# Kernel tuning notes

Hardware: AMD Instinct MI355X
Metric: run time of the kernel (lower is better)

## Reference

```python
import jax, jax.numpy as jnp
import numpy as np


def setup_inputs() -> dict:
    key = jax.random.key(0)
    P, B, S = 128, 128, 4096
    k1, k2, k3, k4 = jax.random.split(key, 4)
    # SPD inducing Gram K_ii
    A = jax.random.normal(k1, (P, 2 * P), jnp.float32)
    K_ii = A @ A.T / (2.0 * P) + 1e-2 * jnp.eye(P, dtype=jnp.float32)
    # cross-covariances [B, S, P]
    K_ti = jax.random.normal(k2, (B, S, P), jnp.float32) * 0.1
    # diagonal K_t must dominate the quadratic form so the Schur complement is positive
    Kii_inv = jnp.linalg.inv(K_ii)
    qf = jnp.einsum('bsp,pq,bsq->bs', K_ti, Kii_inv, K_ti)
    K_t = qf + jax.random.uniform(k3, (B, S), jnp.float32) + 0.1
    # learned parameters
    V = jax.random.normal(k4, (P, P), jnp.float32) / jnp.sqrt(P) + jnp.eye(P, dtype=jnp.float32)
    latent_Gscale = jnp.zeros((), jnp.float32)
    dof = 128
    return dict(K_ii=K_ii, K_ti=K_ti, K_t=K_t, V=V, latent_Gscale=latent_Gscale, dof=dof)


def reference(K_ii, K_ti, K_t, V, latent_Gscale, dof):
    P = K_ii.shape[0]
    ti = K_ti.reshape(-1, P)          # [N, P]
    tt = K_t.reshape(-1)              # [N]
    # pos_inv via Cholesky (SPD inverse)
    L = jnp.linalg.cholesky(K_ii)
    Kii_inv = jax.scipy.linalg.cho_solve((L, True), jnp.eye(P, dtype=K_ii.dtype))
    A = ti @ Kii_inv                  # Kti_inv_Kii_flat, [N, P]
    ktt_i = tt - jnp.sum(A * ti, -1)  # Schur complement diag
    # G = V V^T / P * exp(scale)
    G = (V @ V.T) / V.shape[1] * jnp.exp(latent_Gscale)
    Gti = A @ G                       # [N, P]
    gt = jnp.sum(Gti * A, -1) + ktt_i
    # objective: -0.5 * dof * (-(logdet G + logdet Kinv) + tr(Kinv G) - P)
    trace_term = jnp.sum(Kii_inv * G.T)
    logdet_G = jnp.linalg.slogdet(G)[1]
    logdet_Kinv = -2.0 * jnp.sum(jnp.log(jnp.diag(L)))
    obj = -0.5 * dof * (-(logdet_G + logdet_Kinv) + trace_term - P)
    Gii = G
    return (Gii, Gti.reshape(K_ti.shape), gt.reshape(K_t.shape), obj)
```

## Files before the change

### kernel.cpp

```cpp
#include <hip/hip_runtime.h>
#include <cstdint>

typedef __attribute__((ext_vector_type(8))) short short8;
typedef __attribute__((ext_vector_type(4))) float f32x4;

__device__ __forceinline__ unsigned short f2bf(float f) {
    uint32_t u = __builtin_bit_cast(uint32_t, f);
    u += 0x7FFFu + ((u >> 16) & 1u);
    return (unsigned short)(u >> 16);
}

#define SG_OFF   16384
#define SM1_OFF  32768
#define SY_OFF   49152
#define SX_OFF   65536
#define SD_OFF   81920

__global__ __launch_bounds__(256) void k0_G(
    const float* __restrict__ V, const float* __restrict__ gs,
    float* __restrict__ out)
{
    float* sG = out + SG_OFF;
    const float egs = expf(gs[0]) * (1.0f / 128.0f);
    const int ty = threadIdx.x >> 5, tx = threadIdx.x & 31;
    const int r = blockIdx.x * 8 + ty;
    const f32x4* V4 = (const f32x4*)V;
    f32x4 acc = {0.f, 0.f, 0.f, 0.f};
    for (int kq = 0; kq < 32; ++kq) {
        const f32x4 vr = V4[r * 32 + kq];
        #pragma unroll
        for (int e = 0; e < 4; ++e) {
            const f32x4 vc = V4[(tx * 4 + e) * 32 + kq];
            acc[e] += vr[0]*vc[0] + vr[1]*vc[1] + vr[2]*vc[2] + vr[3]*vc[3];
        }
    }
    acc *= egs;
    *(f32x4*)&out[r * 128 + tx * 4] = acc;
    *(f32x4*)&sG[r * 128 + tx * 4] = acc;
}

__global__ __launch_bounds__(512, 2) void k1_factor(
    const float* __restrict__ Kii, float* __restrict__ out)
{
    __shared__ float colA[2][128], colB[2][128], rowX[2][128];
    __shared__ float sDk[128], sDg[128], sRed[4];

    const int tid = threadIdx.x;
    const int ty = tid >> 5, tx = tid & 31;
    const int I0 = ty * 8, J0 = tx * 4;
    const float* sG = out + SG_OFF;
    float* sX = out + SX_OFF;
    float* dbuf = out + SD_OFF;

    f32x4 rA[8], rB[8], rX[8];
    #pragma unroll
    for (int r = 0; r < 8; ++r) {
        rA[r] = *(const f32x4*)&Kii[(size_t)(I0 + r) * 128 + J0];
        rB[r] = *(const f32x4*)&sG[(I0 + r) * 128 + J0];
        f32x4 z = {0.f, 0.f, 0.f, 0.f};
        #pragma unroll
        for (int e = 0; e < 4; ++e) z[e] = (I0 + r == J0 + e) ? 1.0f : 0.0f;
        rX[r] = z;
    }
    if (tx == 0) {
        #pragma unroll
        for (int r = 0; r < 8; ++r) { colA[0][I0 + r] = rA[r][0]; colB[0][I0 + r] = rB[r][0]; }
    }
    if (ty == 0) {
        #pragma unroll
        for (int e = 0; e < 4; ++e) rowX[0][J0 + e] = rX[0][e];
    }
    __syncthreads();

    for (int k = 0; k < 127; ++k) {
        const int b = k & 1;
        const float dK = colA[b][k], dG = colB[b][k];
        const float rdK = 1.0f / dK, rdG = 1.0f / dG;
        if (tid == 0) { sDk[k] = dK; sDg[k] = dG; }

        f32x4 caj = *(const f32x4*)&colA[b][J0];
        f32x4 cbj = *(const f32x4*)&colB[b][J0];
        const f32x4 xj = *(const f32x4*)&rowX[b][J0];
        #pragma unroll
        for (int e = 0; e < 4; ++e)
            if (J0 + e <= k) { caj[e] = 0.0f; cbj[e] = 0.0f; }

        f32x4 ca0 = *(const f32x4*)&colA[b][I0];
        f32x4 ca1 = *(const f32x4*)&colA[b][I0 + 4];
        f32x4 cb0 = *(const f32x4*)&colB[b][I0];
        f32x4 cb1 = *(const f32x4*)&colB[b][I0 + 4];
        #pragma unroll
        for (int r = 0; r < 4; ++r) {
            if (I0 + r <= k)     { ca0[r] = 0.0f; cb0[r] = 0.0f; }
            if (I0 + 4 + r <= k) { ca1[r] = 0.0f; cb1[r] = 0.0f; }
        }

        if (I0 + 7 > k) {
            #pragma unroll
            for (int r = 0; r < 8; ++r) {
                const float am = (r < 4) ? ca0[r & 3] : ca1[r & 3];
                const float bm = (r < 4) ? cb0[r & 3] : cb1[r & 3];
                const float fA = am * rdK;
                const float fB = bm * rdG;
                rA[r] -= fA * caj;
                rB[r] -= fB * cbj;
                rX[r] -= fA * xj;
            }
        }

        const int kn = k + 1, bn = kn & 1;
        if (tx == (kn >> 2)) {
            const int es = kn & 3;
            #pragma unroll
            for (int ee = 0; ee < 4; ++ee) if (ee == es) {
                #pragma unroll
                for (int r = 0; r < 8; ++r) {
                    colA[bn][I0 + r] = rA[r][ee];
                    colB[bn][I0 + r] = rB[r][ee];
                }
            }
        }
        if (ty == (kn >> 3)) {
            const int rs = kn & 7;
            #pragma unroll
            for (int rr = 0; rr < 8; ++rr) if (rr == rs) {
                #pragma unroll
                for (int e = 0; e < 4; ++e) rowX[bn][J0 + e] = rX[rr][e];
            }
        }
        __syncthreads();
    }
    if (tid == 511) { sDk[127] = rA[7][3]; sDg[127] = rB[7][3]; }

    #pragma unroll
    for (int r = 0; r < 8; ++r)
        *(f32x4*)&sX[(I0 + r) * 128 + J0] = rX[r];
    __syncthreads();

    if (tid < 128) {
        dbuf[tid] = sDk[tid];
        float lk = logf(sDk[tid]);
        float lg = logf(sDg[tid]);
        #pragma unroll
        for (int o = 32; o > 0; o >>= 1) { lk += __shfl_xor(lk, o, 64); lg += __shfl_xor(lg, o, 64); }
        if ((tid & 63) == 0) { sRed[(tid >> 6) * 2] = lk; sRed[(tid >> 6) * 2 + 1] = lg; }
    }
    __syncthreads();
    if (tid == 0) {
        dbuf[128] = sRed[0] + sRed[2];
        dbuf[129] = sRed[1] + sRed[3];
    }
}

__global__ __launch_bounds__(256) void k2_M1(float* __restrict__ out)
{
    const float* sX = out + SX_OFF;
    const float* dbuf = out + SD_OFF;
    float* sM1 = out + SM1_OFF;
    __shared__ float srd[128];
    const int tid = threadIdx.x;
    if (tid < 128) srd[tid] = 1.0f / dbuf[tid];
    __syncthreads();
    const int ty = tid >> 5, tx = tid & 31;
    const int a = blockIdx.x * 8 + ty;
    const f32x4* X4 = (const f32x4*)sX;
    f32x4 acc = {0.f, 0.f, 0.f, 0.f};
    for (int k = a; k < 128; ++k) {
        const float xa = sX[k * 128 + a] * srd[k];
        acc += xa * X4[k * 32 + tx];
    }
    *(f32x4*)&sM1[a * 128 + tx * 4] = acc;
}

__global__ __launch_bounds__(256) void k3_Y(float* __restrict__ out, char* __restrict__ wsb)
{
    const float* sG = out + SG_OFF;
    const float* sM1 = out + SM1_OFF;
    float* sY = out + SY_OFF;
    float* dbuf = out + SD_OFF;
    const int tid = threadIdx.x;
    const int ty = tid >> 5, tx = tid & 31;
    const int c = blockIdx.x * 8 + ty;
    const f32x4* M14 = (const f32x4*)sM1;
    f32x4 acc = {0.f, 0.f, 0.f, 0.f};
    for (int m = 0; m < 128; ++m)
        acc += sG[c * 128 + m] * M14[m * 32 + tx];
    *(f32x4*)&sY[c * 128 + tx * 4] = acc;
    const uint32_t lo = (uint32_t)f2bf(acc[0]) | ((uint32_t)f2bf(acc[1]) << 16);
    const uint32_t hi = (uint32_t)f2bf(acc[2]) | ((uint32_t)f2bf(acc[3]) << 16);
    const uint32_t byteoff = (uint32_t)((c * 256 + tx * 8) ^ ((c & 7) << 4));
    *(uint2*)(wsb + byteoff) = make_uint2(lo, hi);
    float t;
    {
        const f32x4* G4 = (const f32x4*)sG;
        const int idx = blockIdx.x * 256 + tid;
        const f32x4 g = G4[idx], mm = M14[idx];
        t = g[0]*mm[0] + g[1]*mm[1] + g[2]*mm[2] + g[3]*mm[3];
    }
    #pragma unroll
    for (int o = 32; o > 0; o >>= 1) t += __shfl_xor(t, o, 64);
    __shared__ float sp[4];
    if ((tid & 63) == 0) sp[tid >> 6] = t;
    __syncthreads();
    if (tid == 0) dbuf[132 + blockIdx.x] = sp[0] + sp[1] + sp[2] + sp[3];
}

__global__ __launch_bounds__(256) void k4_Q(
    float* __restrict__ out, char* __restrict__ wsb, const int* __restrict__ dofp)
{
    const float* sM1 = out + SM1_OFF;
    const float* sY = out + SY_OFF;
    const float* dbuf = out + SD_OFF;
    const int tid = threadIdx.x;
    const int ty = tid >> 5, tx = tid & 31;
    const int c = blockIdx.x * 8 + ty;
    const f32x4* Y4 = (const f32x4*)sY;
    const f32x4* M14 = (const f32x4*)sM1;
    f32x4 acc = -M14[c * 32 + tx];
    for (int m = 0; m < 128; ++m)
        acc += sM1[c * 128 + m] * Y4[m * 32 + tx];
    const uint32_t lo = (uint32_t)f2bf(acc[0]) | ((uint32_t)f2bf(acc[1]) << 16);
    const uint32_t hi = (uint32_t)f2bf(acc[2]) | ((uint32_t)f2bf(acc[3]) << 16);
    const uint32_t byteoff = (uint32_t)((c * 256 + tx * 8) ^ ((c & 7) << 4));
    *(uint2*)(wsb + 32768 + byteoff) = make_uint2(lo, hi);
    if (blockIdx.x == 0 && tid == 0) {
        float trace = 0.0f;
        for (int i = 0; i < 16; ++i) trace += dbuf[132 + i];
        const float ldK = dbuf[128], ldG = dbuf[129];
        const float dof = (float)dofp[0];
        out[67649536] = -0.5f * dof * (-(ldG - ldK) + trace - 128.0f);
    }
}

__global__ __launch_bounds__(512) void main_kernel(
    const float* __restrict__ Kti, const float* __restrict__ Kt,
    const float* __restrict__ ws, float* __restrict__ Gti,
    float* __restrict__ gt)
{
    __shared__ __align__(16) char smem[65536];
    const int tid = threadIdx.x;
    const int lane = tid & 63, wid = tid >> 6;
    const int l15 = lane & 15, l4 = lane >> 4;
    const int brow = blockIdx.x * 256;
    const int wrow = wid * 32;

    const float* tbase = Kti + (size_t)(brow + wrow + l15) * 128;

    f32x4 t[4][4];
    #pragma unroll
    for (int kc = 0; kc < 4; ++kc) {
        const float* p0 = tbase + kc * 32 + l4 * 8;
        const float* p1 = p0 + 16 * 128;
        t[kc][0] = *(const f32x4*)p0;
        t[kc][1] = *(const f32x4*)(p0 + 4);
        t[kc][2] = *(const f32x4*)p1;
        t[kc][3] = *(const f32x4*)(p1 + 4);
    }

    {
        f32x4* s4 = (f32x4*)smem;
        const f32x4* w4 = (const f32x4*)ws;
        #pragma unroll
        for (int i = 0; i < 8; ++i) s4[tid + i * 512] = w4[tid + i * 512];
    }

    short8 a[4][2];
    #pragma unroll
    for (int kc = 0; kc < 4; ++kc) {
        a[kc][0] = { (short)f2bf(t[kc][0][0]), (short)f2bf(t[kc][0][1]), (short)f2bf(t[kc][0][2]), (short)f2bf(t[kc][0][3]),
                     (short)f2bf(t[kc][1][0]), (short)f2bf(t[kc][1][1]), (short)f2bf(t[kc][1][2]), (short)f2bf(t[kc][1][3]) };
        a[kc][1] = { (short)f2bf(t[kc][2][0]), (short)f2bf(t[kc][2][1]), (short)f2bf(t[kc][2][2]), (short)f2bf(t[kc][2][3]),
                     (short)f2bf(t[kc][3][0]), (short)f2bf(t[kc][3][1]), (short)f2bf(t[kc][3][2]), (short)f2bf(t[kc][3][3]) };
    }
    __syncthreads();

    f32x4 accW[2][8] = {};
    f32x4 accZ[2][8] = {};
    #pragma unroll
    for (int kc = 0; kc < 4; ++kc) {
        const int k0 = kc * 32 + l4 * 8;
        #pragma unroll
        for (int ct = 0; ct < 8; ++ct) {
            const int c = ct * 16 + l15;
            const int byteoff = (c * 256 + k0 * 2) ^ ((c & 7) << 4);
            const short8 bW = *(const short8*)(smem + byteoff);
            const short8 bQ = *(const short8*)(smem + 32768 + byteoff);
            accW[0][ct] = __builtin_amdgcn_mfma_f32_16x16x32_bf16(a[kc][0], bW, accW[0][ct], 0, 0, 0);
            accW[1][ct] = __builtin_amdgcn_mfma_f32_16x16x32_bf16(a[kc][1], bW, accW[1][ct], 0, 0, 0);
            accZ[0][ct] = __builtin_amdgcn_mfma_f32_16x16x32_bf16(a[kc][0], bQ, accZ[0][ct], 0, 0, 0);
            accZ[1][ct] = __builtin_amdgcn_mfma_f32_16x16x32_bf16(a[kc][1], bQ, accZ[1][ct], 0, 0, 0);
        }
    }

    #pragma unroll
    for (int rt = 0; rt < 2; ++rt) {
        #pragma unroll
        for (int r = 0; r < 4; ++r) {
            const int row = brow + wrow + rt * 16 + l4 * 4 + r;
            const float* trow = Kti + (size_t)row * 128;
            float p = 0.0f;
            #pragma unroll
            for (int ct = 0; ct < 8; ++ct) p += accZ[rt][ct][r] * trow[ct * 16 + l15];
            p += __shfl_xor(p, 1, 64);
            p += __shfl_xor(p, 2, 64);
            p += __shfl_xor(p, 4, 64);
            p += __shfl_xor(p, 8, 64);
            if (l15 == 0) gt[row] = Kt[row] + p;
        }
    }

    #pragma unroll
    for (int rt = 0; rt < 2; ++rt) {
        #pragma unroll
        for (int r = 0; r < 4; ++r) {
            float* grow = Gti + (size_t)(brow + wrow + rt * 16 + l4 * 4 + r) * 128 + l15;
            #pragma unroll
            for (int ct = 0; ct < 8; ++ct)
                grow[ct * 16] = accW[rt][ct][r];
        }
    }
}

extern "C" void kernel_launch(void* const* d_in, const int* in_sizes, int n_in,
                              void* d_out, int out_size, void* d_ws, size_t ws_size,
                              hipStream_t stream)
{
    const float* Kii = (const float*)d_in[0];
    const float* Kti = (const float*)d_in[1];
    const float* Kt  = (const float*)d_in[2];
    const float* V   = (const float*)d_in[3];
    const float* gs  = (const float*)d_in[4];
    const int*   dof = (const int*)d_in[5];
    float* out = (float*)d_out;
    float* ws  = (float*)d_ws;

    const int N = in_sizes[2];
    const int nblocks = N / 256;

    k0_G<<<16, 256, 0, stream>>>(V, gs, out);
    k1_factor<<<1, 512, 0, stream>>>(Kii, out);
    k2_M1<<<16, 256, 0, stream>>>(out);
    k3_Y<<<16, 256, 0, stream>>>(out, (char*)ws);
    k4_Q<<<16, 256, 0, stream>>>(out, (char*)ws, dof);
    main_kernel<<<nblocks, 512, 0, stream>>>(Kti, Kt, ws,
                                             out + 16384,
                                             out + 67125248);
}
```

Baseline: 306.2 us.

## Fuse G computation into factor kernel and merge M1/Y/Q kernels into one

Computes G = V V^T scaled inside the single-block factorization kernel, and merges the M1, Y and Q matrix products plus the trace reduction into one 16-block kernel that keeps M1 in shared memory. This removes three kernel launches and the global-memory staging of intermediate matrices. In exchange, each block redundantly recomputes the full M1, and the single-block factor kernel does extra serial work to form G.

```diff
diff --git a/kernel.cpp b/kernel.cpp
--- a/kernel.cpp
+++ b/kernel.cpp
@@ -10,37 +10,12 @@
     return (unsigned short)(u >> 16);
 }
 
-#define SG_OFF   16384
-#define SM1_OFF  32768
-#define SY_OFF   49152
 #define SX_OFF   65536
 #define SD_OFF   81920
 
-__global__ __launch_bounds__(256) void k0_G(
-    const float* __restrict__ V, const float* __restrict__ gs,
-    float* __restrict__ out)
-{
-    float* sG = out + SG_OFF;
-    const float egs = expf(gs[0]) * (1.0f / 128.0f);
-    const int ty = threadIdx.x >> 5, tx = threadIdx.x & 31;
-    const int r = blockIdx.x * 8 + ty;
-    const f32x4* V4 = (const f32x4*)V;
-    f32x4 acc = {0.f, 0.f, 0.f, 0.f};
-    for (int kq = 0; kq < 32; ++kq) {
-        const f32x4 vr = V4[r * 32 + kq];
-        #pragma unroll
-        for (int e = 0; e < 4; ++e) {
-            const f32x4 vc = V4[(tx * 4 + e) * 32 + kq];
-            acc[e] += vr[0]*vc[0] + vr[1]*vc[1] + vr[2]*vc[2] + vr[3]*vc[3];
-        }
-    }
-    acc *= egs;
-    *(f32x4*)&out[r * 128 + tx * 4] = acc;
-    *(f32x4*)&sG[r * 128 + tx * 4] = acc;
-}
-
-__global__ __launch_bounds__(512, 2) void k1_factor(
-    const float* __restrict__ Kii, float* __restrict__ out)
+__global__ __launch_bounds__(512, 2) void kA_factor(
+    const float* __restrict__ Kii, const float* __restrict__ V,
+    const float* __restrict__ gscale, float* __restrict__ out)
 {
     __shared__ float colA[2][128], colB[2][128], rowX[2][128];
     __shared__ float sDk[128], sDg[128], sRed[4];
@@ -48,15 +23,39 @@
     const int tid = threadIdx.x;
     const int ty = tid >> 5, tx = tid & 31;
     const int I0 = ty * 8, J0 = tx * 4;
-    const float* sG = out + SG_OFF;
     float* sX = out + SX_OFF;
     float* dbuf = out + SD_OFF;
 
-    f32x4 rA[8], rB[8], rX[8];
+    f32x4 rB[8];
+    {
+        const float egs = expf(gscale[0]) * (1.0f / 128.0f);
+        const f32x4* V4 = (const f32x4*)V;
+        float acc[8][4] = {};
+        for (int q = 0; q < 32; ++q) {
+            f32x4 vc[4];
+            #pragma unroll
+            for (int e = 0; e < 4; ++e) vc[e] = V4[(J0 + e) * 32 + q];
+            #pragma unroll
+            for (int r = 0; r < 8; ++r) {
+                const f32x4 vr = V4[(I0 + r) * 32 + q];
+                #pragma unroll
+                for (int e = 0; e < 4; ++e)
+                    acc[r][e] += vr[0]*vc[e][0] + vr[1]*vc[e][1]
+                               + vr[2]*vc[e][2] + vr[3]*vc[e][3];
+            }
+        }
+        #pragma unroll
+        for (int r = 0; r < 8; ++r) {
+            const f32x4 g = { acc[r][0]*egs, acc[r][1]*egs, acc[r][2]*egs, acc[r][3]*egs };
+            rB[r] = g;
+            *(f32x4*)&out[(I0 + r) * 128 + J0] = g;
+        }
+    }
+
+    f32x4 rA[8], rX[8];
     #pragma unroll
     for (int r = 0; r < 8; ++r) {
         rA[r] = *(const f32x4*)&Kii[(size_t)(I0 + r) * 128 + J0];
-        rB[r] = *(const f32x4*)&sG[(I0 + r) * 128 + J0];
         f32x4 z = {0.f, 0.f, 0.f, 0.f};
         #pragma unroll
         for (int e = 0; e < 4; ++e) z[e] = (I0 + r == J0 + e) ? 1.0f : 0.0f;
@@ -152,83 +151,96 @@
     }
 }
 
-__global__ __launch_bounds__(256) void k2_M1(float* __restrict__ out)
-{
-    const float* sX = out + SX_OFF;
-    const float* dbuf = out + SD_OFF;
-    float* sM1 = out + SM1_OFF;
-    __shared__ float srd[128];
-    const int tid = threadIdx.x;
-    if (tid < 128) srd[tid] = 1.0f / dbuf[tid];
-    __syncthreads();
-    const int ty = tid >> 5, tx = tid & 31;
-    const int a = blockIdx.x * 8 + ty;
-    const f32x4* X4 = (const f32x4*)sX;
-    f32x4 acc = {0.f, 0.f, 0.f, 0.f};
-    for (int k = a; k < 128; ++k) {
-        const float xa = sX[k * 128 + a] * srd[k];
-        acc += xa * X4[k * 32 + tx];
-    }
-    *(f32x4*)&sM1[a * 128 + tx * 4] = acc;
-}
-
-__global__ __launch_bounds__(256) void k3_Y(float* __restrict__ out, char* __restrict__ wsb)
-{
-    const float* sG = out + SG_OFF;
-    const float* sM1 = out + SM1_OFF;
-    float* sY = out + SY_OFF;
-    float* dbuf = out + SD_OFF;
-    const int tid = threadIdx.x;
-    const int ty = tid >> 5, tx = tid & 31;
-    const int c = blockIdx.x * 8 + ty;
-    const f32x4* M14 = (const f32x4*)sM1;
-    f32x4 acc = {0.f, 0.f, 0.f, 0.f};
-    for (int m = 0; m < 128; ++m)
-        acc += sG[c * 128 + m] * M14[m * 32 + tx];
-    *(f32x4*)&sY[c * 128 + tx * 4] = acc;
-    const uint32_t lo = (uint32_t)f2bf(acc[0]) | ((uint32_t)f2bf(acc[1]) << 16);
-    const uint32_t hi = (uint32_t)f2bf(acc[2]) | ((uint32_t)f2bf(acc[3]) << 16);
-    const uint32_t byteoff = (uint32_t)((c * 256 + tx * 8) ^ ((c & 7) << 4));
-    *(uint2*)(wsb + byteoff) = make_uint2(lo, hi);
-    float t;
-    {
-        const f32x4* G4 = (const f32x4*)sG;
-        const int idx = blockIdx.x * 256 + tid;
-        const f32x4 g = G4[idx], mm = M14[idx];
-        t = g[0]*mm[0] + g[1]*mm[1] + g[2]*mm[2] + g[3]*mm[3];
-    }
-    #pragma unroll
-    for (int o = 32; o > 0; o >>= 1) t += __shfl_xor(t, o, 64);
-    __shared__ float sp[4];
-    if ((tid & 63) == 0) sp[tid >> 6] = t;
-    __syncthreads();
-    if (tid == 0) dbuf[132 + blockIdx.x] = sp[0] + sp[1] + sp[2] + sp[3];
-}
-
-__global__ __launch_bounds__(256) void k4_Q(
+__global__ __launch_bounds__(256) void kG_rest(
     float* __restrict__ out, char* __restrict__ wsb, const int* __restrict__ dofp)
 {
-    const float* sM1 = out + SM1_OFF;
-    const float* sY = out + SY_OFF;
+    __shared__ float M1s[128 * 132];
+    __shared__ float Zs[8 * 132];
+    __shared__ float srd[128];
+
+    const int tid = threadIdx.x;
+    const int bid = blockIdx.x;
+    const float* Xg = out + SX_OFF;
     const float* dbuf = out + SD_OFF;
-    const int tid = threadIdx.x;
-    const int ty = tid >> 5, tx = tid & 31;
-    const int c = blockIdx.x * 8 + ty;
-    const f32x4* Y4 = (const f32x4*)sY;
-    const f32x4* M14 = (const f32x4*)sM1;
-    f32x4 acc = -M14[c * 32 + tx];
-    for (int m = 0; m < 128; ++m)
-        acc += sM1[c * 128 + m] * Y4[m * 32 + tx];
-    const uint32_t lo = (uint32_t)f2bf(acc[0]) | ((uint32_t)f2bf(acc[1]) << 16);
-    const uint32_t hi = (uint32_t)f2bf(acc[2]) | ((uint32_t)f2bf(acc[3]) << 16);
-    const uint32_t byteoff = (uint32_t)((c * 256 + tx * 8) ^ ((c & 7) << 4));
-    *(uint2*)(wsb + 32768 + byteoff) = make_uint2(lo, hi);
-    if (blockIdx.x == 0 && tid == 0) {
-        float trace = 0.0f;
-        for (int i = 0; i < 16; ++i) trace += dbuf[132 + i];
-        const float ldK = dbuf[128], ldG = dbuf[129];
-        const float dof = (float)dofp[0];
-        out[67649536] = -0.5f * dof * (-(ldG - ldK) + trace - 128.0f);
+    const float* G = out;
+
+    if (tid < 128) srd[tid] = 1.0f / dbuf[tid];
+    __syncthreads();
+
+    {
+        const int ty = tid >> 5, tx = tid & 31;
+        const int I0 = ty * 16, J0 = tx * 4;
+        f32x4 acc[16] = {};
+        for (int k = 0; k < 128; ++k) {
+            f32x4 xb = *(const f32x4*)&Xg[k * 128 + J0];
+            xb *= srd[k];
+            const f32x4 xa0 = *(const f32x4*)&Xg[k * 128 + I0];
+            const f32x4 xa1 = *(const f32x4*)&Xg[k * 128 + I0 + 4];
+            const f32x4 xa2 = *(const f32x4*)&Xg[k * 128 + I0 + 8];
+            const f32x4 xa3 = *(const f32x4*)&Xg[k * 128 + I0 + 12];
+            #pragma unroll
+            for (int r = 0; r < 4; ++r) {
+                acc[r]      += xa0[r] * xb;
+                acc[r + 4]  += xa1[r] * xb;
+                acc[r + 8]  += xa2[r] * xb;
+                acc[r + 12] += xa3[r] * xb;
+            }
+        }
+        #pragma unroll
+        for (int r = 0; r < 16; ++r)
+            *(f32x4*)&M1s[(I0 + r) * 132 + J0] = acc[r];
+    }
+    __syncthreads();
+
+    const int r8 = tid >> 5;
+    const int j4 = tid & 31;
+    const int c = bid * 8 + r8;
+
+    {
+        f32x4 y = {0.f, 0.f, 0.f, 0.f};
+        const float* grow = G + (size_t)c * 128;
+        for (int m = 0; m < 128; ++m)
+            y += grow[m] * *(const f32x4*)&M1s[m * 132 + j4 * 4];
+        const uint32_t lo = (uint32_t)f2bf(y[0]) | ((uint32_t)f2bf(y[1]) << 16);
+        const uint32_t hi = (uint32_t)f2bf(y[2]) | ((uint32_t)f2bf(y[3]) << 16);
+        const uint32_t byteoff = (uint32_t)((c * 256 + j4 * 8) ^ ((c & 7) << 4));
+        *(uint2*)(wsb + byteoff) = make_uint2(lo, hi);
+    }
+
+    float trp = 0.0f;
+    {
+        f32x4 z = {0.f, 0.f, 0.f, 0.f};
+        const f32x4* G4 = (const f32x4*)G;
+        for (int m = 0; m < 128; ++m) {
+            const f32x4 g = G4[m * 32 + j4];
+            z += M1s[c * 132 + m] * g;
+            if (r8 == 0) {
+                const f32x4 mm = *(const f32x4*)&M1s[m * 132 + j4 * 4];
+                trp += mm[0]*g[0] + mm[1]*g[1] + mm[2]*g[2] + mm[3]*g[3];
+            }
+        }
+        *(f32x4*)&Zs[r8 * 132 + j4 * 4] = z;
+    }
+    __syncthreads();
+
+    {
+        f32x4 q = - *(const f32x4*)&M1s[c * 132 + j4 * 4];
+        for (int m = 0; m < 128; ++m)
+            q += Zs[r8 * 132 + m] * *(const f32x4*)&M1s[m * 132 + j4 * 4];
+        const uint32_t lo = (uint32_t)f2bf(q[0]) | ((uint32_t)f2bf(q[1]) << 16);
+        const uint32_t hi = (uint32_t)f2bf(q[2]) | ((uint32_t)f2bf(q[3]) << 16);
+        const uint32_t byteoff = (uint32_t)((c * 256 + j4 * 8) ^ ((c & 7) << 4));
+        *(uint2*)(wsb + 32768 + byteoff) = make_uint2(lo, hi);
+    }
+
+    if (r8 == 0) {
+        #pragma unroll
+        for (int o = 16; o > 0; o >>= 1) trp += __shfl_xor(trp, o, 32);
+        if (tid == 0 && bid == 0) {
+            const float ldK = dbuf[128], ldG = dbuf[129];
+            const float dof = (float)dofp[0];
+            out[67649536] = -0.5f * dof * (-(ldG - ldK) + trp - 128.0f);
+        }
     }
 }
 
@@ -337,11 +349,8 @@
     const int N = in_sizes[2];
     const int nblocks = N / 256;
 
-    k0_G<<<16, 256, 0, stream>>>(V, gs, out);
-    k1_factor<<<1, 512, 0, stream>>>(Kii, out);
-    k2_M1<<<16, 256, 0, stream>>>(out);
-    k3_Y<<<16, 256, 0, stream>>>(out, (char*)ws);
-    k4_Q<<<16, 256, 0, stream>>>(out, (char*)ws, dof);
+    kA_factor<<<1, 512, 0, stream>>>(Kii, V, gs, out);
+    kG_rest<<<16, 256, 0, stream>>>(out, (char*)ws, dof);
     main_kernel<<<nblocks, 512, 0, stream>>>(Kti, Kt, ws,
                                              out + 16384,
                                              out + 67125248);
```

After: 350.1 us. 1.14x slower.

## Block the LDL factorization and split K and G factorizations across two blocks

Applied to the files above, without the earlier changes.

Replaces the 127-step rank-1 elimination loop in the single-block factor kernel with a 16-wide blocked LDL^T scheme. Each panel is factored in shared memory, the trailing matrix gets a rank-16 update, and only about 24 barriers remain instead of 127. The K_ii and G factorizations now run in two separate blocks rather than interleaved in one. The serial single-block stage should get shorter, but panel factorization runs on a single wavefront and there is more shared-memory traffic.

```diff
diff --git a/kernel.cpp b/kernel.cpp
--- a/kernel.cpp
+++ b/kernel.cpp
@@ -39,117 +39,156 @@
     *(f32x4*)&sG[r * 128 + tx * 4] = acc;
 }
 
-__global__ __launch_bounds__(512, 2) void k1_factor(
+__global__ __launch_bounds__(512, 2) void k1b_factor(
     const float* __restrict__ Kii, float* __restrict__ out)
 {
-    __shared__ float colA[2][128], colB[2][128], rowX[2][128];
-    __shared__ float sDk[128], sDg[128], sRed[4];
-
-    const int tid = threadIdx.x;
+    __shared__ float PR[128 * 17];
+    __shared__ float PS[128 * 17];
+    __shared__ float PRT[16 * 132];
+    __shared__ float XP[16 * 132];
+    __shared__ float sD[128], sRed[2];
+
+    const int tid = threadIdx.x;
+    const int wv = tid >> 6;
+    const int lane = tid & 63;
     const int ty = tid >> 5, tx = tid & 31;
     const int I0 = ty * 8, J0 = tx * 4;
-    const float* sG = out + SG_OFF;
-    float* sX = out + SX_OFF;
+    const bool isK = (blockIdx.x == 0);
+    const float* src = isK ? Kii : (out + SG_OFF);
     float* dbuf = out + SD_OFF;
 
-    f32x4 rA[8], rB[8], rX[8];
+    f32x4 rA[8], rX[8];
     #pragma unroll
     for (int r = 0; r < 8; ++r) {
-        rA[r] = *(const f32x4*)&Kii[(size_t)(I0 + r) * 128 + J0];
-        rB[r] = *(const f32x4*)&sG[(I0 + r) * 128 + J0];
+        rA[r] = *(const f32x4*)&src[(size_t)(I0 + r) * 128 + J0];
         f32x4 z = {0.f, 0.f, 0.f, 0.f};
         #pragma unroll
         for (int e = 0; e < 4; ++e) z[e] = (I0 + r == J0 + e) ? 1.0f : 0.0f;
         rX[r] = z;
     }
-    if (tx == 0) {
-        #pragma unroll
-        for (int r = 0; r < 8; ++r) { colA[0][I0 + r] = rA[r][0]; colB[0][I0 + r] = rB[r][0]; }
-    }
-    if (ty == 0) {
-        #pragma unroll
-        for (int e = 0; e < 4; ++e) rowX[0][J0 + e] = rX[0][e];
+
+    for (int kb = 0; kb < 128; kb += 16) {
+        if (J0 >= kb && J0 < kb + 16) {
+            const int c0 = J0 - kb;
+            #pragma unroll
+            for (int r = 0; r < 8; ++r) {
+                #pragma unroll
+                for (int e = 0; e < 4; ++e)
+                    PR[(I0 + r) * 17 + c0 + e] = rA[r][e];
+            }
+        }
+        if (isK && I0 >= kb && I0 < kb + 16) {
+            #pragma unroll
+            for (int r = 0; r < 8; ++r)
+                *(f32x4*)&XP[(I0 + r - kb) * 132 + J0] = rX[r];
+        }
+        __syncthreads();
+
+        if (wv == 0) {
+            const int di = lane & 15;
+            const int m4 = (lane >> 4) * 4;
+            #pragma unroll
+            for (int p = 0; p < 16; ++p) {
+                const float d = PR[(kb + p) * 17 + p];
+                if (lane == 0) sD[kb + p] = d;
+                const float rdp = 1.0f / d;
+                const float aip = PR[(kb + di) * 17 + p];
+                float pm[4];
+                #pragma unroll
+                for (int e = 0; e < 4; ++e) pm[e] = PR[(kb + p) * 17 + m4 + e];
+                #pragma unroll
+                for (int e = 0; e < 4; ++e)
+                    if (di > p && (m4 + e) > p)
+                        PR[(kb + di) * 17 + m4 + e] -= aip * pm[e] * rdp;
+            }
+        }
+        __syncthreads();
+
+        if (wv < 2) {
+            const int i = kb + 16 + wv * 64 + lane;
+            if (i < 128) {
+                float rdv[16], pr[16];
+                #pragma unroll
+                for (int m = 0; m < 16; ++m) {
+                    rdv[m] = 1.0f / sD[kb + m];
+                    pr[m] = PR[i * 17 + m];
+                }
+                #pragma unroll
+                for (int j = 1; j < 16; ++j) {
+                    #pragma unroll
+                    for (int m = 0; m < 16; ++m)
+                        if (m < j)
+                            pr[j] -= pr[m] * PR[(kb + j) * 17 + m] * rdv[m];
+                }
+                #pragma unroll
+                for (int m = 0; m < 16; ++m) {
+                    PR[i * 17 + m] = pr[m];
+                    PRT[m * 132 + i] = pr[m];
+                    PS[i * 17 + m] = pr[m] * rdv[m];
+                }
+            }
+        } else if (wv == 2 && isK) {
+            const int c0 = lane * 2;
+            #pragma unroll
+            for (int p = 1; p < 16; ++p) {
+                float x0 = XP[p * 132 + c0], x1 = XP[p * 132 + c0 + 1];
+                #pragma unroll
+                for (int m = 0; m < 16; ++m) {
+                    if (m < p) {
+                        const float f = PR[(kb + p) * 17 + m] * (1.0f / sD[kb + m]);
+                        x0 -= f * XP[m * 132 + c0];
+                        x1 -= f * XP[m * 132 + c0 + 1];
+                    }
+                }
+                XP[p * 132 + c0] = x0;
+                XP[p * 132 + c0 + 1] = x1;
+            }
+        }
+        __syncthreads();
+
+        const bool rowOK = (I0 >= kb + 16);
+        const bool colOK = (J0 >= kb + 16);
+        if (rowOK) {
+            #pragma unroll
+            for (int m = 0; m < 16; ++m) {
+                float si[8];
+                #pragma unroll
+                for (int r = 0; r < 8; ++r) si[r] = PS[(I0 + r) * 17 + m];
+                if (isK) {
+                    const f32x4 xv = *(const f32x4*)&XP[m * 132 + J0];
+                    #pragma unroll
+                    for (int r = 0; r < 8; ++r) rX[r] -= si[r] * xv;
+                }
+                if (colOK) {
+                    const f32x4 cj = *(const f32x4*)&PRT[m * 132 + J0];
+                    #pragma unroll
+                    for (int r = 0; r < 8; ++r) rA[r] -= si[r] * cj;
+                }
+            }
+        }
+        if (isK && I0 >= kb && I0 < kb + 16) {
+            #pragma unroll
+            for (int r = 0; r < 8; ++r)
+                rX[r] = *(const f32x4*)&XP[(I0 + r - kb) * 132 + J0];
+        }
+        __syncthreads();
+    }
+
+    if (isK) {
+        float* sXg = out + SX_OFF;
+        #pragma unroll
+        for (int r = 0; r < 8; ++r)
+            *(f32x4*)&sXg[(I0 + r) * 128 + J0] = rX[r];
+    }
+    if (tid < 128) {
+        if (isK) dbuf[tid] = sD[tid];
+        float lv = logf(sD[tid]);
+        #pragma unroll
+        for (int o = 32; o > 0; o >>= 1) lv += __shfl_xor(lv, o, 64);
+        if ((tid & 63) == 0) sRed[tid >> 6] = lv;
     }
     __syncthreads();
-
-    for (int k = 0; k < 127; ++k) {
-        const int b = k & 1;
-        const float dK = colA[b][k], dG = colB[b][k];
-        const float rdK = 1.0f / dK, rdG = 1.0f / dG;
-        if (tid == 0) { sDk[k] = dK; sDg[k] = dG; }
-
-        f32x4 caj = *(const f32x4*)&colA[b][J0];
-        f32x4 cbj = *(const f32x4*)&colB[b][J0];
-        const f32x4 xj = *(const f32x4*)&rowX[b][J0];
-        #pragma unroll
-        for (int e = 0; e < 4; ++e)
-            if (J0 + e <= k) { caj[e] = 0.0f; cbj[e] = 0.0f; }
-
-        f32x4 ca0 = *(const f32x4*)&colA[b][I0];
-        f32x4 ca1 = *(const f32x4*)&colA[b][I0 + 4];
-        f32x4 cb0 = *(const f32x4*)&colB[b][I0];
-        f32x4 cb1 = *(const f32x4*)&colB[b][I0 + 4];
-        #pragma unroll
-        for (int r = 0; r < 4; ++r) {
-            if (I0 + r <= k)     { ca0[r] = 0.0f; cb0[r] = 0.0f; }
-            if (I0 + 4 + r <= k) { ca1[r] = 0.0f; cb1[r] = 0.0f; }
-        }
-
-        if (I0 + 7 > k) {
-            #pragma unroll
-            for (int r = 0; r < 8; ++r) {
-                const float am = (r < 4) ? ca0[r & 3] : ca1[r & 3];
-                const float bm = (r < 4) ? cb0[r & 3] : cb1[r & 3];
-                const float fA = am * rdK;
-                const float fB = bm * rdG;
-                rA[r] -= fA * caj;
-                rB[r] -= fB * cbj;
-                rX[r] -= fA * xj;
-            }
-        }
-
-        const int kn = k + 1, bn = kn & 1;
-        if (tx == (kn >> 2)) {
-            const int es = kn & 3;
-            #pragma unroll
-            for (int ee = 0; ee < 4; ++ee) if (ee == es) {
-                #pragma unroll
-                for (int r = 0; r < 8; ++r) {
-                    colA[bn][I0 + r] = rA[r][ee];
-                    colB[bn][I0 + r] = rB[r][ee];
-                }
-            }
-        }
-        if (ty == (kn >> 3)) {
-            const int rs = kn & 7;
-            #pragma unroll
-            for (int rr = 0; rr < 8; ++rr) if (rr == rs) {
-                #pragma unroll
-                for (int e = 0; e < 4; ++e) rowX[bn][J0 + e] = rX[rr][e];
-            }
-        }
-        __syncthreads();
-    }
-    if (tid == 511) { sDk[127] = rA[7][3]; sDg[127] = rB[7][3]; }
-
-    #pragma unroll
-    for (int r = 0; r < 8; ++r)
-        *(f32x4*)&sX[(I0 + r) * 128 + J0] = rX[r];
-    __syncthreads();
-
-    if (tid < 128) {
-        dbuf[tid] = sDk[tid];
-        float lk = logf(sDk[tid]);
-        float lg = logf(sDg[tid]);
-        #pragma unroll
-        for (int o = 32; o > 0; o >>= 1) { lk += __shfl_xor(lk, o, 64); lg += __shfl_xor(lg, o, 64); }
-        if ((tid & 63) == 0) { sRed[(tid >> 6) * 2] = lk; sRed[(tid >> 6) * 2 + 1] = lg; }
-    }
-    __syncthreads();
-    if (tid == 0) {
-        dbuf[128] = sRed[0] + sRed[2];
-        dbuf[129] = sRed[1] + sRed[3];
-    }
+    if (tid == 0) dbuf[isK ? 128 : 129] = sRed[0] + sRed[1];
 }
 
 __global__ __launch_bounds__(256) void k2_M1(float* __restrict__ out)
@@ -338,7 +377,7 @@
     const int nblocks = N / 256;
 
     k0_G<<<16, 256, 0, stream>>>(V, gs, out);
-    k1_factor<<<1, 512, 0, stream>>>(Kii, out);
+    k1b_factor<<<2, 512, 0, stream>>>(Kii, out);
     k2_M1<<<16, 256, 0, stream>>>(out);
     k3_Y<<<16, 256, 0, stream>>>(out, (char*)ws);
     k4_Q<<<16, 256, 0, stream>>>(out, (char*)ws, dof);
```

New measurement: 311.9 us. About the same (+1.9%).
